# Kernel optimization log

Hardware: AMD Instinct MI355X
Metric: run time of the kernel (lower is better)

## Reference

```python
import jax, jax.numpy as jnp
import numpy as np

N = 12288
E = 393216
IN = 64
OUT = 64
EPS = 1e-8


def setup_inputs() -> dict:
    key = jax.random.key(0)
    k1, k2, k3, k4, k5 = jax.random.split(key, 5)
    x = jax.random.normal(k1, (N, IN), dtype=jnp.float32)
    edge_index = jax.random.randint(k2, (2, E), 0, N, dtype=jnp.int32)
    W_self = jax.random.normal(k3, (OUT, IN), dtype=jnp.float32) / np.sqrt(IN)
    W_neigh = jax.random.normal(k4, (OUT, IN), dtype=jnp.float32) / np.sqrt(IN)
    bound = 1.0 / np.sqrt(IN)
    bias = jax.random.uniform(k5, (OUT,), dtype=jnp.float32, minval=-bound, maxval=bound)
    return {"x": x, "edge_index": edge_index, "W_self": W_self, "W_neigh": W_neigh, "bias": bias}


def _proj_norm(p):
    # normalize feature part, keep homogeneous coordinate
    feat = p[..., :-1]
    norm = jnp.linalg.norm(feat, axis=-1, keepdims=True)
    return jnp.concatenate([feat / (norm + EPS), p[..., -1:]], axis=-1)


def _proj_transform(x, W):
    # x: [N, in+1], W: [out, in] -> [N, out+1]
    feat = x[..., :-1] @ W.T
    return _proj_norm(jnp.concatenate([feat, x[..., -1:]], axis=-1))


def _proj_average(points, weights):
    # points: [K, ..., D], weights: [K]
    avg = jnp.einsum('k,k...->...', weights, points)
    return _proj_norm(avg)


def _forward(x, edge_index, W_self, W_neigh, bias):
    xh = jnp.concatenate([x, jnp.ones_like(x[..., :1])], axis=-1)  # [N, in+1]
    self_trans = _proj_transform(xh, W_self)  # [N, out+1]

    # --- aggregate_neighbors ---
    row, col = edge_index[0], edge_index[1]
    all_nodes = _proj_transform(xh, W_neigh)  # [N, out+1]
    n = xh.shape[0]
    adj = jnp.zeros((n, n), jnp.float32).at[row, col].set(1.0) + jnp.eye(n, dtype=jnp.float32)
    # per-edge cross-ratio weight (symmetric in src/dst)
    xf = xh[..., :-1]
    ps, pd = xf[row], xf[col]  # [E, in]
    cos = jnp.sum(ps * pd, axis=-1) / (
        jnp.linalg.norm(ps, axis=-1) * jnp.linalg.norm(pd, axis=-1) + EPS)
    w = jnp.clip((cos + 1.0) * 0.5, 0.1, 0.9)  # [E]
    adj = adj.at[row, col].set(w).at[col, row].set(w)
    adj = adj / (adj.sum(axis=1, keepdims=True) + EPS)
    neigh_trans = _proj_norm(adj @ all_nodes)  # [N, out+1]

    # --- combine self and neighbor, then bias ---
    out = _proj_average(jnp.stack([self_trans, neigh_trans]),
                        jnp.array([0.5, 0.5], jnp.float32))
    bp = jnp.concatenate([bias, jnp.ones_like(bias[:1])])
    bp = bp / jnp.linalg.norm(bp)
    out = _proj_average(jnp.stack([out, jnp.broadcast_to(bp, out.shape)]),
                        jnp.array([0.9, 0.1], jnp.float32))
    feat = out[..., :-1]
    return feat / (jnp.linalg.norm(feat, axis=-1, keepdims=True) + EPS)


def reference(x, edge_index, W_self, W_neigh, bias):
    return _forward(x, edge_index, W_self, W_neigh, bias)
```

## Files before the change

kernel.cpp:

```cpp
#include <hip/hip_runtime.h>
#include <math.h>

#define N_NODES 12288
#define N_EDGES 393216
#define DIM 64
#define EPS 1e-8f
#define SLOTS 192

__device__ __forceinline__ float wave_sum(float v) {
    #pragma unroll
    for (int off = 32; off; off >>= 1) v += __shfl_xor(v, off);
    return v;
}

__global__ __launch_bounds__(256) void phase1_kernel(
    const float* __restrict__ x, const float* __restrict__ Wself,
    const float* __restrict__ Wneigh,
    float* __restrict__ s_norm, float* __restrict__ anf) {
    __shared__ float Wl[2 * 64 * 65];
    const int tid = threadIdx.x;

    #pragma unroll
    for (int v = 0; v < 4; ++v) {
        const int idx4 = v * 256 + tid;
        const int o = idx4 >> 4, k4 = (idx4 & 15) << 2;
        const float4 a = *(const float4*)&Wself[idx4 << 2];
        Wl[o * 65 + k4 + 0] = a.x; Wl[o * 65 + k4 + 1] = a.y;
        Wl[o * 65 + k4 + 2] = a.z; Wl[o * 65 + k4 + 3] = a.w;
        const float4 b = *(const float4*)&Wneigh[idx4 << 2];
        float* W2 = &Wl[64 * 65];
        W2[o * 65 + k4 + 0] = b.x; W2[o * 65 + k4 + 1] = b.y;
        W2[o * 65 + k4 + 2] = b.z; W2[o * 65 + k4 + 3] = b.w;
    }
    __syncthreads();

    const int o = tid & 63;
    const int i = blockIdx.x * 4 + (tid >> 6);
    const float* xr = &x[(size_t)i * 64];

    float ys = 0.f, yn = 0.f;
    #pragma unroll
    for (int t = 0; t < 16; ++t) {
        const float4 xv = *(const float4*)&xr[4 * t];
        const int kb = 4 * t;
        ys = fmaf(xv.x, Wl[o * 65 + kb + 0], ys);
        ys = fmaf(xv.y, Wl[o * 65 + kb + 1], ys);
        ys = fmaf(xv.z, Wl[o * 65 + kb + 2], ys);
        ys = fmaf(xv.w, Wl[o * 65 + kb + 3], ys);
        yn = fmaf(xv.x, Wl[64 * 65 + o * 65 + kb + 0], yn);
        yn = fmaf(xv.y, Wl[64 * 65 + o * 65 + kb + 1], yn);
        yn = fmaf(xv.z, Wl[64 * 65 + o * 65 + kb + 2], yn);
        yn = fmaf(xv.w, Wl[64 * 65 + o * 65 + kb + 3], yn);
    }

    const float nys = sqrtf(wave_sum(ys * ys));
    const float nyn = sqrtf(wave_sum(yn * yn));
    s_norm[(size_t)i * 64 + o] = ys / (nys + EPS);
    anf[(size_t)i * 64 + o]    = yn / (nyn + EPS);
}

__global__ __launch_bounds__(256) void edge_scatter_kernel(
    const float* __restrict__ x, const int* __restrict__ ei,
    int* __restrict__ deg, int2* __restrict__ meta) {
    const int lane = threadIdx.x & 63;
    const int j = lane & 7;
    const int wave = blockIdx.x * 4 + (threadIdx.x >> 6);
    const int e = wave * 8 + (lane >> 3);

    const int r = ei[e];
    const int c = ei[N_EDGES + e];

    const size_t rb = (size_t)r * 64 + j * 8;
    const size_t cb = (size_t)c * 64 + j * 8;
    const float4 xr0 = *(const float4*)&x[rb];
    const float4 xr1 = *(const float4*)&x[rb + 4];
    const float4 xc0 = *(const float4*)&x[cb];
    const float4 xc1 = *(const float4*)&x[cb + 4];

    float p = xr0.x*xc0.x + xr0.y*xc0.y + xr0.z*xc0.z + xr0.w*xc0.w
            + xr1.x*xc1.x + xr1.y*xc1.y + xr1.z*xc1.z + xr1.w*xc1.w;
    float nr = xr0.x*xr0.x + xr0.y*xr0.y + xr0.z*xr0.z + xr0.w*xr0.w
             + xr1.x*xr1.x + xr1.y*xr1.y + xr1.z*xr1.z + xr1.w*xr1.w;
    float nc = xc0.x*xc0.x + xc0.y*xc0.y + xc0.z*xc0.z + xc0.w*xc0.w
             + xc1.x*xc1.x + xc1.y*xc1.y + xc1.z*xc1.z + xc1.w*xc1.w;
    #pragma unroll
    for (int off = 1; off < 8; off <<= 1) {
        p  += __shfl_xor(p,  off);
        nr += __shfl_xor(nr, off);
        nc += __shfl_xor(nc, off);
    }

    const float cosv = p / (sqrtf(nr) * sqrtf(nc) + EPS);
    float w = fminf(fmaxf((cosv + 1.0f) * 0.5f, 0.1f), 0.9f);
    const float wv = (r == c) ? (w - 1.0f) : w;
    const int wbits = __float_as_int(wv);

    if (j == 0) {
        int s = atomicAdd(&deg[r], 1);
        if (s < SLOTS) meta[(size_t)r * SLOTS + s] = make_int2(c, wbits);
    } else if (j == 1) {
        int s = atomicAdd(&deg[c], 1);
        if (s < SLOTS) meta[(size_t)c * SLOTS + s] = make_int2(r, wbits);
    }
}

__global__ __launch_bounds__(256) void gather_finalize_kernel(
    const int* __restrict__ deg, const int2* __restrict__ meta,
    const float* __restrict__ anf, const float* __restrict__ s_norm,
    const float* __restrict__ bias, float* __restrict__ out) {
    __shared__ int2 cw[4][SLOTS];
    const int lane = threadIdx.x & 63;
    const int w4 = threadIdx.x >> 6;
    const int i = blockIdx.x * 4 + w4;

    const int d = min(deg[i], SLOTS);

    int2 m0 = make_int2(-1, 0), m1 = make_int2(-1, 0), m2 = make_int2(-1, 0);
    if (lane < d)       { m0 = meta[(size_t)i * SLOTS + lane];       cw[w4][lane]       = m0; }
    if (lane + 64 < d)  { m1 = meta[(size_t)i * SLOTS + lane + 64];  cw[w4][lane + 64]  = m1; }
    if (lane + 128 < d) { m2 = meta[(size_t)i * SLOTS + lane + 128]; cw[w4][lane + 128] = m2; }
    __syncthreads();

    int dup0 = 0, dup1 = 0, dup2 = 0;
    for (int s = 0; s < d; ++s) {
        const int cs = cw[w4][s].x;
        dup0 |= (s < lane)       & (cs == m0.x);
        dup1 |= (s < lane + 64)  & (cs == m1.x);
        dup2 |= (s < lane + 128) & (cs == m2.x);
    }

    float Sp = 0.f;
    if (lane < d)       { if (dup0) cw[w4][lane].y       = 0; else Sp += __int_as_float(m0.y); }
    if (lane + 64 < d)  { if (dup1) cw[w4][lane + 64].y  = 0; else Sp += __int_as_float(m1.y); }
    if (lane + 128 < d) { if (dup2) cw[w4][lane + 128].y = 0; else Sp += __int_as_float(m2.y); }
    const float S = 1.0f + wave_sum(Sp);
    __syncthreads();

    float acc = anf[(size_t)i * 64 + lane];
    #pragma unroll 8
    for (int k = 0; k < d; ++k) {
        const int2 ent = cw[w4][k];
        acc = fmaf(__int_as_float(ent.y), anf[(size_t)ent.x * 64 + lane], acc);
    }

    const float v = acc / (S + EPS);
    const float nv = sqrtf(wave_sum(v * v));
    const float nf = v / (nv + EPS);

    const float s = s_norm[(size_t)i * 64 + lane];
    const float h = 0.5f * (s + nf);
    const float nh = sqrtf(wave_sum(h * h));
    const float hf = h / (nh + EPS);

    const float bd = bias[lane];
    const float nb = sqrtf(wave_sum(bd * bd) + 1.0f);
    const float g = 0.9f * hf + 0.1f * (bd / nb);
    const float ng = sqrtf(wave_sum(g * g));
    const float gf = g / (ng + EPS);

    const float rho = ng / (ng + EPS);
    out[(size_t)i * 64 + lane] = gf / (rho + EPS);
}

extern "C" void kernel_launch(void* const* d_in, const int* in_sizes, int n_in,
                              void* d_out, int out_size, void* d_ws, size_t ws_size,
                              hipStream_t stream) {
    const float* x      = (const float*)d_in[0];
    const int*   ei     = (const int*)  d_in[1];
    const float* Wself  = (const float*)d_in[2];
    const float* Wneigh = (const float*)d_in[3];
    const float* bias   = (const float*)d_in[4];
    float* out = (float*)d_out;

    const size_t ROW_BYTES = (size_t)N_NODES * 64 * sizeof(float);
    char* ws = (char*)d_ws;
    int*  deg    = (int*)ws;      ws += (size_t)N_NODES * sizeof(int);
    int2* meta   = (int2*)ws;     ws += (size_t)N_NODES * SLOTS * sizeof(int2);
    float* s_norm = (float*)ws;   ws += ROW_BYTES;
    float* anf    = (float*)ws;   ws += ROW_BYTES;

    hipMemsetAsync(deg, 0, (size_t)N_NODES * sizeof(int), stream);

    edge_scatter_kernel<<<N_EDGES / 8 / 4, 256, 0, stream>>>(x, ei, deg, meta);

    phase1_kernel<<<N_NODES / 4, 256, 0, stream>>>(x, Wself, Wneigh,
                                                   s_norm, anf);

    gather_finalize_kernel<<<N_NODES / 4, 256, 0, stream>>>(deg, meta, anf,
                                                            s_norm, bias, out);
}
```

Before: 157.7 us.

## Bin edges per node group and XCD, deduplicate with shared bitmaps

Replaces the per-node atomic slot lists with coarse bins of 12 nodes, each split into per-XCD sub-bins. This cuts contention on global atomics and keeps each atomic counter local to one XCD's L2. The gather kernel merges the sub-bins into a shared-memory CSR and removes duplicate edges with atomicOr on a per-node bitmap, replacing the quadratic pairwise duplicate scan. Risks: sub-bin capacity (256) or per-node slot (128) overflow drops edges, and only 1024 blocks do the gather, which lowers parallelism.

```diff
diff --git a/kernel.cpp b/kernel.cpp
--- a/kernel.cpp
+++ b/kernel.cpp
@@ -3,9 +3,15 @@
 
 #define N_NODES 12288
 #define N_EDGES 393216
-#define DIM 64
 #define EPS 1e-8f
-#define SLOTS 192
+
+#define NB 1024
+#define NPB 12
+#define NXCD 8
+#define NSUB (NB * NXCD)
+#define CAP_SUB 256
+#define NSLOT 128
+#define BMW 384
 
 __device__ __forceinline__ float wave_sum(float v) {
     #pragma unroll
@@ -19,7 +25,6 @@
     float* __restrict__ s_norm, float* __restrict__ anf) {
     __shared__ float Wl[2 * 64 * 65];
     const int tid = threadIdx.x;
-
     #pragma unroll
     for (int v = 0; v < 4; ++v) {
         const int idx4 = v * 256 + tid;
@@ -59,9 +64,9 @@
     anf[(size_t)i * 64 + o]    = yn / (nyn + EPS);
 }
 
-__global__ __launch_bounds__(256) void edge_scatter_kernel(
+__global__ __launch_bounds__(256) void edge_bin_kernel(
     const float* __restrict__ x, const int* __restrict__ ei,
-    int* __restrict__ deg, int2* __restrict__ meta) {
+    int* __restrict__ subcnt, int2* __restrict__ buf) {
     const int lane = threadIdx.x & 63;
     const int j = lane & 7;
     const int wave = blockIdx.x * 4 + (threadIdx.x >> 6);
@@ -95,71 +100,93 @@
     const float wv = (r == c) ? (w - 1.0f) : w;
     const int wbits = __float_as_int(wv);
 
-    if (j == 0) {
-        int s = atomicAdd(&deg[r], 1);
-        if (s < SLOTS) meta[(size_t)r * SLOTS + s] = make_int2(c, wbits);
-    } else if (j == 1) {
-        int s = atomicAdd(&deg[c], 1);
-        if (s < SLOTS) meta[(size_t)c * SLOTS + s] = make_int2(r, wbits);
-    }
-}
-
-__global__ __launch_bounds__(256) void gather_finalize_kernel(
-    const int* __restrict__ deg, const int2* __restrict__ meta,
+    int xcc;
+    asm volatile("s_getreg_b32 %0, hwreg(20, 0, 4)" : "=s"(xcc));
+    xcc &= 7;
+
+    if (j < 2) {
+        const int dest = j ? c : r;
+        const int col  = j ? r : c;
+        const int sub = (dest / NPB) * NXCD + xcc;
+        const int s = atomicAdd(&subcnt[sub], 1);
+        if (s < CAP_SUB)
+            buf[(size_t)sub * CAP_SUB + s] = make_int2((dest << 14) | col, wbits);
+    }
+}
+
+__global__ __launch_bounds__(256) void bin_gather_kernel(
+    const int* __restrict__ subcnt, const int2* __restrict__ buf,
     const float* __restrict__ anf, const float* __restrict__ s_norm,
     const float* __restrict__ bias, float* __restrict__ out) {
-    __shared__ int2 cw[4][SLOTS];
-    const int lane = threadIdx.x & 63;
-    const int w4 = threadIdx.x >> 6;
-    const int i = blockIdx.x * 4 + w4;
-
-    const int d = min(deg[i], SLOTS);
-
-    int2 m0 = make_int2(-1, 0), m1 = make_int2(-1, 0), m2 = make_int2(-1, 0);
-    if (lane < d)       { m0 = meta[(size_t)i * SLOTS + lane];       cw[w4][lane]       = m0; }
-    if (lane + 64 < d)  { m1 = meta[(size_t)i * SLOTS + lane + 64];  cw[w4][lane + 64]  = m1; }
-    if (lane + 128 < d) { m2 = meta[(size_t)i * SLOTS + lane + 128]; cw[w4][lane + 128] = m2; }
+    __shared__ int2 csr[NPB][NSLOT];
+    __shared__ unsigned bm[NPB * BMW];
+    __shared__ int cnt[NPB];
+    const int tid = threadIdx.x;
+    const int lane = tid & 63;
+    const int w4 = tid >> 6;
+    const int bin = blockIdx.x;
+    const int node0 = bin * NPB;
+
+    for (int t = tid; t < NPB * BMW; t += 256) bm[t] = 0u;
+    if (tid < NPB) cnt[tid] = 0;
     __syncthreads();
 
-    int dup0 = 0, dup1 = 0, dup2 = 0;
-    for (int s = 0; s < d; ++s) {
-        const int cs = cw[w4][s].x;
-        dup0 |= (s < lane)       & (cs == m0.x);
-        dup1 |= (s < lane + 64)  & (cs == m1.x);
-        dup2 |= (s < lane + 128) & (cs == m2.x);
-    }
-
-    float Sp = 0.f;
-    if (lane < d)       { if (dup0) cw[w4][lane].y       = 0; else Sp += __int_as_float(m0.y); }
-    if (lane + 64 < d)  { if (dup1) cw[w4][lane + 64].y  = 0; else Sp += __int_as_float(m1.y); }
-    if (lane + 128 < d) { if (dup2) cw[w4][lane + 128].y = 0; else Sp += __int_as_float(m2.y); }
-    const float S = 1.0f + wave_sum(Sp);
+    for (int xc = 0; xc < NXCD; ++xc) {
+        const int sub = bin * NXCD + xc;
+        const int n = min(subcnt[sub], CAP_SUB);
+        const int2* seg = &buf[(size_t)sub * CAP_SUB];
+        for (int t = tid; t < n; t += 256) {
+            const int2 rec = seg[t];
+            const int dest = rec.x >> 14;
+            const int col  = rec.x & 16383;
+            const int l = dest - node0;
+            const unsigned bit = 1u << (col & 31);
+            const unsigned old = atomicOr(&bm[l * BMW + (col >> 5)], bit);
+            if (!(old & bit)) {
+                const int s = atomicAdd(&cnt[l], 1);
+                if (s < NSLOT) csr[l][s] = make_int2(col, rec.y);
+            }
+        }
+    }
     __syncthreads();
-
-    float acc = anf[(size_t)i * 64 + lane];
-    #pragma unroll 8
-    for (int k = 0; k < d; ++k) {
-        const int2 ent = cw[w4][k];
-        acc = fmaf(__int_as_float(ent.y), anf[(size_t)ent.x * 64 + lane], acc);
-    }
-
-    const float v = acc / (S + EPS);
-    const float nv = sqrtf(wave_sum(v * v));
-    const float nf = v / (nv + EPS);
-
-    const float s = s_norm[(size_t)i * 64 + lane];
-    const float h = 0.5f * (s + nf);
-    const float nh = sqrtf(wave_sum(h * h));
-    const float hf = h / (nh + EPS);
 
     const float bd = bias[lane];
     const float nb = sqrtf(wave_sum(bd * bd) + 1.0f);
-    const float g = 0.9f * hf + 0.1f * (bd / nb);
-    const float ng = sqrtf(wave_sum(g * g));
-    const float gf = g / (ng + EPS);
-
-    const float rho = ng / (ng + EPS);
-    out[(size_t)i * 64 + lane] = gf / (rho + EPS);
+    const float bterm = 0.1f * (bd / nb);
+
+    #pragma unroll 1
+    for (int q = 0; q < 3; ++q) {
+        const int l = w4 * 3 + q;
+        const int i = node0 + l;
+        const int d = min(cnt[l], NSLOT);
+
+        float acc = anf[(size_t)i * 64 + lane];
+        #pragma unroll 4
+        for (int k = 0; k < d; ++k) {
+            const int2 ent = csr[l][k];
+            acc = fmaf(__int_as_float(ent.y), anf[(size_t)ent.x * 64 + lane], acc);
+        }
+        float Sp = 0.f;
+        if (lane < d)      Sp += __int_as_float(csr[l][lane].y);
+        if (lane + 64 < d) Sp += __int_as_float(csr[l][lane + 64].y);
+        const float S = 1.0f + wave_sum(Sp);
+
+        const float v = acc / (S + EPS);
+        const float nv = sqrtf(wave_sum(v * v));
+        const float nf = v / (nv + EPS);
+
+        const float s = s_norm[(size_t)i * 64 + lane];
+        const float h = 0.5f * (s + nf);
+        const float nh = sqrtf(wave_sum(h * h));
+        const float hf = h / (nh + EPS);
+
+        const float g = 0.9f * hf + bterm;
+        const float ng = sqrtf(wave_sum(g * g));
+        const float gf = g / (ng + EPS);
+
+        const float rho = ng / (ng + EPS);
+        out[(size_t)i * 64 + lane] = gf / (rho + EPS);
+    }
 }
 
 extern "C" void kernel_launch(void* const* d_in, const int* in_sizes, int n_in,
@@ -174,18 +201,18 @@
 
     const size_t ROW_BYTES = (size_t)N_NODES * 64 * sizeof(float);
     char* ws = (char*)d_ws;
-    int*  deg    = (int*)ws;      ws += (size_t)N_NODES * sizeof(int);
-    int2* meta   = (int2*)ws;     ws += (size_t)N_NODES * SLOTS * sizeof(int2);
-    float* s_norm = (float*)ws;   ws += ROW_BYTES;
-    float* anf    = (float*)ws;   ws += ROW_BYTES;
-
-    hipMemsetAsync(deg, 0, (size_t)N_NODES * sizeof(int), stream);
-
-    edge_scatter_kernel<<<N_EDGES / 8 / 4, 256, 0, stream>>>(x, ei, deg, meta);
+    int*  subcnt = (int*)ws;   ws += (size_t)NSUB * sizeof(int);
+    int2* buf    = (int2*)ws;  ws += (size_t)NSUB * CAP_SUB * sizeof(int2);
+    float* s_norm = (float*)ws; ws += ROW_BYTES;
+    float* anf    = (float*)ws; ws += ROW_BYTES;
+
+    hipMemsetAsync(subcnt, 0, (size_t)NSUB * sizeof(int), stream);
+
+    edge_bin_kernel<<<N_EDGES / 8 / 4, 256, 0, stream>>>(x, ei, subcnt, buf);
 
     phase1_kernel<<<N_NODES / 4, 256, 0, stream>>>(x, Wself, Wneigh,
                                                    s_norm, anf);
 
-    gather_finalize_kernel<<<N_NODES / 4, 256, 0, stream>>>(deg, meta, anf,
-                                                            s_norm, bias, out);
-}
+    bin_gather_kernel<<<NB, 256, 0, stream>>>(subcnt, buf, anf, s_norm,
+                                              bias, out);
+}
```

Result: faster. 140.2 us (-11.1%).
